# Kernel tuning notes

Hardware: AMD Instinct MI355X
Metric: run time of the kernel (lower is better)

Reference implementation:

```python
import jax, jax.numpy as jnp
import numpy as np

VOCAB, D_MODEL, N_STATE, H_HEADS, LAYERS = 64, 512, 32, 16, 4
EXPAND = 2
D_INNER = EXPAND * D_MODEL          # 1024
P_HEAD = D_INNER // H_HEADS         # 64
CONV_DIM = D_INNER + 2 * N_STATE    # x, B, C share the depthwise conv
K_CONV = 4
D_IN_PROJ = 2 * D_INNER + 2 * N_STATE + H_HEADS  # z, x, B, C, dt
BATCH, SEQ = 4, 1024
EPS = 1e-5


def rmsnorm(x, w):
    return x * jax.lax.rsqrt(jnp.mean(x * x, axis=-1, keepdims=True) + EPS) * w


def silu(x):
    return x * jax.nn.sigmoid(x)


def causal_depthwise_conv(x, w, b):
    # x: [B,L,C], w: [C,K], b: [C]; causal (left) padding, depthwise groups
    xt = jnp.transpose(x, (0, 2, 1))  # [B,C,L]
    out = jax.lax.conv_general_dilated(xt, w[:, None, :], (1,), [(K_CONV - 1, 0)], feature_group_count=w.shape[0])
    return jnp.transpose(out, (0, 2, 1)) + b


def ssd(xh, dt, A, Bm, Cm, Dp):
    # Mamba2 SSD recurrence. xh [B,L,H,P], dt [B,L,H], A [H], Bm/Cm [B,L,N], Dp [H]
    dA = jnp.exp(dt * A)              # decay per (batch, step, head)
    dtx = dt[..., None] * xh          # [B,L,H,P]

    def step(h, inp):
        dA_t, dtx_t, B_t, C_t = inp
        # h: [B,H,P,N]
        h = dA_t[:, :, None, None] * h + dtx_t[..., None] * B_t[:, None, None, :]
        y = jnp.einsum('bhpn,bn->bhp', h, C_t)
        return h, y

    h0 = jnp.zeros((xh.shape[0], H_HEADS, P_HEAD, N_STATE), xh.dtype)
    _, ys = jax.lax.scan(step, h0, (jnp.moveaxis(dA, 1, 0), jnp.moveaxis(dtx, 1, 0), jnp.moveaxis(Bm, 1, 0), jnp.moveaxis(Cm, 1, 0)))
    return jnp.moveaxis(ys, 0, 1) + xh * Dp[None, None, :, None]


def mamba_block(x, norm_w, W_in, b_in, conv_w, conv_b, dt_bias, A_log, Dp, gnorm_w, W_out, b_out):
    res = x
    u = rmsnorm(x, norm_w)
    zxbcdt = u @ W_in + b_in                                # [B,L,D_IN_PROJ]
    z = zxbcdt[..., :D_INNER]
    xBC = zxbcdt[..., D_INNER:D_INNER + CONV_DIM]
    dt = zxbcdt[..., D_INNER + CONV_DIM:]                   # [B,L,H]
    xBC = silu(causal_depthwise_conv(xBC, conv_w, conv_b))
    xc = xBC[..., :D_INNER]
    Bm = xBC[..., D_INNER:D_INNER + N_STATE]
    Cm = xBC[..., D_INNER + N_STATE:]
    dt = jax.nn.softplus(dt + dt_bias)
    xh = xc.reshape(xc.shape[0], xc.shape[1], H_HEADS, P_HEAD)
    y = ssd(xh, dt, -jnp.exp(A_log), Bm, Cm, Dp)
    y = y.reshape(y.shape[0], y.shape[1], D_INNER)
    y = rmsnorm(y * silu(z), gnorm_w)                       # gated RMSNorm
    return res + y @ W_out + b_out


def forward(input_tokens, emb, norm_w, W_in, b_in, conv_w, conv_b, dt_bias, A_log, D_param, gnorm_w, W_out, b_out, head_w, head_b):
    h = emb[input_tokens]
    for i in range(LAYERS):
        h = mamba_block(h, norm_w[i], W_in[i], b_in[i], conv_w[i], conv_b[i], dt_bias[i], A_log[i], D_param[i], gnorm_w[i], W_out[i], b_out[i])
    return h @ head_w + head_b


def setup_inputs() -> dict:
    key = jax.random.key(0)
    ks = jax.random.split(key, 8)
    s = 0.02
    return {
        'input_tokens': jax.random.randint(ks[0], (BATCH, SEQ), 0, VOCAB),
        'emb': jax.random.normal(ks[1], (VOCAB, D_MODEL), jnp.float32) * s,
        'norm_w': jnp.ones((LAYERS, D_MODEL), jnp.float32),
        'W_in': jax.random.normal(ks[2], (LAYERS, D_MODEL, D_IN_PROJ), jnp.float32) * s,
        'b_in': jnp.zeros((LAYERS, D_IN_PROJ), jnp.float32),
        'conv_w': jax.random.normal(ks[3], (LAYERS, CONV_DIM, K_CONV), jnp.float32) * 0.1,
        'conv_b': jnp.zeros((LAYERS, CONV_DIM), jnp.float32),
        'dt_bias': jnp.tile(jnp.log(jnp.expm1(jnp.linspace(0.001, 0.1, H_HEADS, dtype=jnp.float32))), (LAYERS, 1)),
        'A_log': jnp.tile(jnp.log(jnp.arange(1, H_HEADS + 1, dtype=jnp.float32)), (LAYERS, 1)),
        'D_param': jnp.ones((LAYERS, H_HEADS), jnp.float32),
        'gnorm_w': jnp.ones((LAYERS, D_INNER), jnp.float32),
        'W_out': jax.random.normal(ks[4], (LAYERS, D_INNER, D_MODEL), jnp.float32) * s,
        'b_out': jnp.zeros((LAYERS, D_MODEL), jnp.float32),
        'head_w': jax.random.normal(ks[5], (D_MODEL, VOCAB), jnp.float32) * s,
        'head_b': jnp.zeros((VOCAB,), jnp.float32),
    }


def reference(input_tokens, emb, norm_w, W_in, b_in, conv_w, conv_b, dt_bias, A_log, D_param, gnorm_w, W_out, b_out, head_w, head_b):
    return forward(input_tokens, emb, norm_w, W_in, b_in, conv_w, conv_b, dt_bias, A_log, D_param, gnorm_w, W_out, b_out, head_w, head_b)
```

## Files before the change

### kernel.cpp

```cpp
#include <hip/hip_runtime.h>
#include <hip/hip_bf16.h>

#define VOCAB     64
#define D_MODEL   512
#define N_STATE   32
#define H_HEADS   16
#define LAYERS    4
#define D_INNER   1024
#define P_HEAD    64
#define CONV_DIM  1088
#define K_CONV    4
#define D_IN_PROJ 2128
#define NPAD_IN   2176
#define NPAD_HEAD 64
#define BATCH     4
#define SEQ       1024
#define NTOK      (BATCH*SEQ)
#define EPS       1e-5f
#define CL        64
#define NC        (SEQ/CL)
#define PSTR      80

typedef __bf16 bf16x8 __attribute__((ext_vector_type(8)));
typedef float  f32x4  __attribute__((ext_vector_type(4)));

__device__ __forceinline__ float sigmoidf_(float x) { return 1.f / (1.f + __expf(-x)); }
__device__ __forceinline__ float softplusf_(float x) { return (x > 20.f) ? x : log1pf(__expf(x)); }

__device__ __forceinline__ void gload_lds16(const void* g, void* l) {
  __builtin_amdgcn_global_load_lds((const __attribute__((address_space(1))) void*)g,
                                   (__attribute__((address_space(3))) void*)l,
                                   16, 0, 0);
}

__device__ __forceinline__ int xcd_lin() {
  return (blockIdx.x & 7) * ((int)gridDim.x >> 3) + ((int)blockIdx.x >> 3);
}

__global__ __launch_bounds__(256) void embed_kernel(
    const int* __restrict__ tok, const float* __restrict__ emb,
    float* __restrict__ h, __bf16* __restrict__ hbf) {
  int wv = threadIdx.x >> 6, lane = threadIdx.x & 63;
  int tokid = blockIdx.x * 4 + wv;
  const float* er = emb + (size_t)tok[tokid] * D_MODEL;
  f32x4 v0 = *(const f32x4*)(er + lane * 8);
  f32x4 v1 = *(const f32x4*)(er + lane * 8 + 4);
  float* hr = h + (size_t)tokid * D_MODEL;
  *(f32x4*)(hr + lane * 8) = v0;
  *(f32x4*)(hr + lane * 8 + 4) = v1;
  bf16x8 o8;
  #pragma unroll
  for (int k = 0; k < 4; k++) { o8[k] = (__bf16)v0[k]; o8[4 + k] = (__bf16)v1[k]; }
  *(bf16x8*)(hbf + (size_t)tokid * D_MODEL + lane * 8) = o8;
}

__global__ __launch_bounds__(256) void transpose_all_kernel(
    const float* __restrict__ W_in, const float* __restrict__ W_out,
    const float* __restrict__ head_w,
    const float* __restrict__ norm_w, const float* __restrict__ gnorm_w,
    __bf16* __restrict__ WtIn, __bf16* __restrict__ WtOut, __bf16* __restrict__ WtHead) {
  int b = blockIdx.x;
  const float* W; const float* fold; __bf16* Wt; int K, N, Npad, bx, by;
  if (b < 4352) {
    int z = b / 1088, r = b % 1088;
    bx = r % 68; by = r / 68;
    W = W_in + (size_t)z * D_MODEL * D_IN_PROJ;
    fold = norm_w + (size_t)z * D_MODEL;
    Wt = WtIn + (size_t)z * NPAD_IN * D_MODEL;
    K = D_MODEL; N = D_IN_PROJ; Npad = NPAD_IN;
  } else if (b < 6400) {
    int r = b - 4352; int z = r / 512; r %= 512;
    bx = r % 16; by = r / 16;
    W = W_out + (size_t)z * D_INNER * D_MODEL;
    fold = gnorm_w + (size_t)z * D_INNER;
    Wt = WtOut + (size_t)z * D_MODEL * D_INNER;
    K = D_INNER; N = D_MODEL; Npad = D_MODEL;
  } else {
    int r = b - 6400;
    bx = r % 2; by = r / 2;
    W = head_w; fold = nullptr; Wt = WtHead;
    K = D_MODEL; N = VOCAB; Npad = NPAD_HEAD;
  }
  __shared__ float T[32][33];
  int n0 = bx * 32, k0 = by * 32;
  int tx = threadIdx.x & 31, ty = threadIdx.x >> 5;
  #pragma unroll
  for (int i = 0; i < 4; i++) {
    int n = n0 + tx;
    T[ty + i * 8][tx] = (n < N) ? W[(size_t)(k0 + ty + i * 8) * N + n] : 0.f;
  }
  __syncthreads();
  float fs = fold ? fold[k0 + tx] : 1.f;
  #pragma unroll
  for (int i = 0; i < 4; i++)
    Wt[(size_t)(n0 + ty + i * 8) * K + k0 + tx] = (__bf16)(T[tx][ty + i * 8] * fs);
}

#define TK 64
__global__ __launch_bounds__(256) void gemm64_kernel(
    const __bf16* __restrict__ A, const __bf16* __restrict__ Bt,
    const float* __restrict__ bias, const float* __restrict__ res,
    float* __restrict__ C, __bf16* __restrict__ Cbf,
    float inv_norm_dim, int nbx, int K, int N, int ldc) {
  __shared__ __bf16 As[2][64 * TK];
  __shared__ __bf16 Bs[2][64 * TK];
  int tid = threadIdx.x;
  int lane = tid & 63, wave = tid >> 6;
  int wm = wave >> 1, wn = wave & 1;
  int q = lane >> 4, l16 = lane & 15;
  int lin = xcd_lin();
  int bx = lin % nbx, by = lin / nbx;
  size_t row0 = (size_t)by * 64;
  int col0 = bx * 64;
  const __bf16* Ab = A + row0 * K;
  const __bf16* Bb = Bt + (size_t)col0 * K;

  auto stage = [&](int buf, int kk) {
    #pragma unroll
    for (int r = 0; r < 2; r++) {
      int lin2 = r * 256 + tid;
      size_t goff = (size_t)(lin2 >> 3) * K + kk + (lin2 & 7) * 8;
      gload_lds16(Ab + goff, &As[buf][lin2 * 8]);
      gload_lds16(Bb + goff, &Bs[buf][lin2 * 8]);
    }
  };

  f32x4 acc[2][2];
  #pragma unroll
  for (int i = 0; i < 2; i++)
    #pragma unroll
    for (int j = 0; j < 2; j++) acc[i][j] = (f32x4){0.f, 0.f, 0.f, 0.f};
  float ssqa[2] = {0.f, 0.f};

  stage(0, 0);
  int cur = 0;
  for (int k0 = 0; k0 < K; k0 += TK) {
    if (k0 + TK < K) {
      stage(cur ^ 1, k0 + TK);
      asm volatile("s_waitcnt vmcnt(4)" ::: "memory");
    } else {
      asm volatile("s_waitcnt vmcnt(0)" ::: "memory");
    }
    __builtin_amdgcn_s_barrier();
    #pragma unroll
    for (int ks = 0; ks < 2; ks++) {
      bf16x8 af[2], bfv[2];
      #pragma unroll
      for (int i = 0; i < 2; i++) {
        af[i] = *(const bf16x8*)(&As[cur][(wm * 32 + i * 16 + l16) * TK + ks * 32 + q * 8]);
        #pragma unroll
        for (int k = 0; k < 8; k++) { float v = (float)af[i][k]; ssqa[i] += v * v; }
      }
      #pragma unroll
      for (int j = 0; j < 2; j++)
        bfv[j] = *(const bf16x8*)(&Bs[cur][(wn * 32 + j * 16 + l16) * TK + ks * 32 + q * 8]);
      #pragma unroll
      for (int i = 0; i < 2; i++)
        #pragma unroll
        for (int j = 0; j < 2; j++)
          acc[i][j] = __builtin_amdgcn_mfma_f32_16x16x32_bf16(af[i], bfv[j], acc[i][j], 0, 0, 0);
    }
    __builtin_amdgcn_s_barrier();
    cur ^= 1;
  }

  #pragma unroll
  for (int i = 0; i < 2; i++) {
    ssqa[i] += __shfl_xor(ssqa[i], 16);
    ssqa[i] += __shfl_xor(ssqa[i], 32);
  }
  #pragma unroll
  for (int i = 0; i < 2; i++) {
    #pragma unroll
    for (int rr = 0; rr < 4; rr++) {
      size_t mrow = row0 + wm * 32 + i * 16 + q * 4 + rr;
      float sq = __shfl(ssqa[i], q * 4 + rr);
      float sc = (inv_norm_dim > 0.f) ? rsqrtf(sq * inv_norm_dim + EPS) : 1.f;
      #pragma unroll
      for (int j = 0; j < 2; j++) {
        int col = col0 + wn * 32 + j * 16 + l16;
        if (col < N) {
          size_t off = mrow * (size_t)ldc + col;
          float v = acc[i][j][rr] * sc + (bias ? bias[col] : 0.f);
          if (res) v += res[off];
          if (C)   C[off] = v;
          if (Cbf) Cbf[off] = (__bf16)v;
        }
      }
    }
  }
}

__global__ __launch_bounds__(256) void gemm_in_kernel(
    const __bf16* __restrict__ A, const __bf16* __restrict__ Bt,
    const float* __restrict__ bias, __bf16* __restrict__ Cbf,
    int nbx, int K, int N, int ldc) {
  __shared__ __bf16 As[2][64 * TK];
  __shared__ __bf16 Bs[2][128 * TK];
  int tid = threadIdx.x;
  int lane = tid & 63, wave = tid >> 6;
  int wm = wave >> 1, wn = wave & 1;
  int q = lane >> 4, l16 = lane & 15;
  int lin = xcd_lin();
  int bx = lin % nbx, by = lin / nbx;
  size_t row0 = (size_t)by * 64;
  int col0 = bx * 128;
  const __bf16* Ab = A + row0 * K;
  const __bf16* Bb = Bt + (size_t)col0 * K;

  auto stage = [&](int buf, int kk) {
    #pragma unroll
    for (int r = 0; r < 2; r++) {
      int lin2 = r * 256 + tid;
      gload_lds16(Ab + (size_t)(lin2 >> 3) * K + kk + (lin2 & 7) * 8, &As[buf][lin2 * 8]);
    }
    #pragma unroll
    for (int r = 0; r < 4; r++) {
      int lin2 = r * 256 + tid;
      gload_lds16(Bb + (size_t)(lin2 >> 3) * K + kk + (lin2 & 7) * 8, &Bs[buf][lin2 * 8]);
    }
  };

  f32x4 acc[2][4];
  #pragma unroll
  for (int i = 0; i < 2; i++)
    #pragma unroll
    for (int j = 0; j < 4; j++) acc[i][j] = (f32x4){0.f, 0.f, 0.f, 0.f};
  float ssqa[2] = {0.f, 0.f};

  stage(0, 0);
  int cur = 0;
  for (int k0 = 0; k0 < K; k0 += TK) {
    if (k0 + TK < K) {
      stage(cur ^ 1, k0 + TK);
      asm volatile("s_waitcnt vmcnt(6)" ::: "memory");
    } else {
      asm volatile("s_waitcnt vmcnt(0)" ::: "memory");
    }
    __builtin_amdgcn_s_barrier();
    #pragma unroll
    for (int ks = 0; ks < 2; ks++) {
      bf16x8 af[2], bfv[4];
      #pragma unroll
      for (int i = 0; i < 2; i++) {
        af[i] = *(const bf16x8*)(&As[cur][(wm * 32 + i * 16 + l16) * TK + ks * 32 + q * 8]);
        #pragma unroll
        for (int k = 0; k < 8; k++) { float v = (float)af[i][k]; ssqa[i] += v * v; }
      }
      #pragma unroll
      for (int j = 0; j < 4; j++)
        bfv[j] = *(const bf16x8*)(&Bs[cur][(wn * 64 + j * 16 + l16) * TK + ks * 32 + q * 8]);
      #pragma unroll
      for (int i = 0; i < 2; i++)
        #pragma unroll
        for (int j = 0; j < 4; j++)
          acc[i][j] = __builtin_amdgcn_mfma_f32_16x16x32_bf16(af[i], bfv[j], acc[i][j], 0, 0, 0);
    }
    __builtin_amdgcn_s_barrier();
    cur ^= 1;
  }

  #pragma unroll
  for (int i = 0; i < 2; i++) {
    ssqa[i] += __shfl_xor(ssqa[i], 16);
    ssqa[i] += __shfl_xor(ssqa[i], 32);
  }
  #pragma unroll
  for (int i = 0; i < 2; i++) {
    #pragma unroll
    for (int rr = 0; rr < 4; rr++) {
      size_t mrow = row0 + wm * 32 + i * 16 + q * 4 + rr;
      float sq = __shfl(ssqa[i], q * 4 + rr);
      float sc = rsqrtf(sq * (1.f / D_MODEL) + EPS);
      #pragma unroll
      for (int j = 0; j < 4; j++) {
        int col = col0 + wn * 64 + j * 16 + l16;
        if (col < N)
          Cbf[mrow * (size_t)ldc + col] = (__bf16)(acc[i][j][rr] * sc + bias[col]);
      }
    }
  }
}

__device__ __forceinline__ void wave0_dt_cumsum(
    const __bf16* __restrict__ zxbf, const float* __restrict__ dt_bias,
    int b, int h, int t0, int tid, float* ldt, float* lcs) {
  if (tid < 64) {
    float dv = (float)zxbf[((size_t)(b * SEQ + t0 + tid)) * D_IN_PROJ + 2 * D_INNER + 2 * N_STATE + h]
               + dt_bias[h];
    float dtv = softplusf_(dv);
    float cs = dtv;
    #pragma unroll
    for (int off = 1; off < 64; off <<= 1) {
      float o = __shfl_up(cs, off);
      if (tid >= off) cs += o;
    }
    ldt[tid] = dtv;
    lcs[tid] = cs;
  }
}

__global__ __launch_bounds__(256) void ssd_local_kernel(
    const __bf16* __restrict__ zxbf, const float* __restrict__ conv_w,
    const float* __restrict__ conv_b, const float* __restrict__ dt_bias,
    const float* __restrict__ A_log,
    float* __restrict__ Slocal, float* __restrict__ dAprod) {
  int blk = xcd_lin();
  int c = blk % NC;
  int h = (blk / NC) % H_HEADS;
  int b = blk / (NC * H_HEADS);
  int tid = threadIdx.x;
  int lane = tid & 63, wave = tid >> 6;
  int q = lane >> 4, l16 = lane & 15;
  int t0 = c * CL;
  float A = -__expf(A_log[h]);
  __shared__ __bf16 rawbuf[68 * 64 + 68 * 32];
  __shared__ __bf16 lxT[64][PSTR];
  __shared__ __bf16 lBT[32][PSTR];
  __shared__ float ldt[64], lcs[64];
  __bf16* rawx = rawbuf;
  __bf16* rawB = rawbuf + 68 * 64;
  for (int i = tid; i < 68 * 8; i += 256) {
    int r = i >> 3, c0 = (i & 7) * 8;
    int gr = t0 - 3 + r;
    bf16x8 v;
    #pragma unroll
    for (int k = 0; k < 8; k++) v[k] = (__bf16)0.f;
    if (gr >= 0)
      v = *(const bf16x8*)(zxbf + ((size_t)(b * SEQ + gr)) * D_IN_PROJ + D_INNER + h * 64 + c0);
    *(bf16x8*)(rawx + r * 64 + c0) = v;
  }
  for (int i = tid; i < 68 * 4; i += 256) {
    int r = i >> 2, c0 = (i & 3) * 8;
    int gr = t0 - 3 + r;
    bf16x8 v;
    #pragma unroll
    for (int k = 0; k < 8; k++) v[k] = (__bf16)0.f;
    if (gr >= 0)
      v = *(const bf16x8*)(zxbf + ((size_t)(b * SEQ + gr)) * D_IN_PROJ + 2 * D_INNER + c0);
    *(bf16x8*)(rawB + r * 32 + c0) = v;
  }
  wave0_dt_cumsum(zxbf, dt_bias, b, h, t0, tid, ldt, lcs);
  __syncthreads();
  float cs63 = lcs[63];
  {
    int p = tid & 63;
    const float* w = conv_w + (h * 64 + p) * K_CONV;
    float w0 = w[0], w1 = w[1], w2 = w[2], w3 = w[3];
    float cb = conv_b[h * 64 + p];
    for (int i = tid; i < CL * 64; i += 256) {
      int t = i >> 6;
      float a = cb + w0 * (float)rawx[t * 64 + p] + w1 * (float)rawx[(t + 1) * 64 + p]
                   + w2 * (float)rawx[(t + 2) * 64 + p] + w3 * (float)rawx[(t + 3) * 64 + p];
      lxT[p][t] = (__bf16)(a * sigmoidf_(a));
    }
  }
  {
    int n = tid & 31;
    const float* w = conv_w + (D_INNER + n) * K_CONV;
    float w0 = w[0], w1 = w[1], w2 = w[2], w3 = w[3];
    float cb = conv_b[D_INNER + n];
    for (int i = tid; i < CL * 32; i += 256) {
      int t = i >> 5;
      float a = cb + w0 * (float)rawB[t * 32 + n] + w1 * (float)rawB[(t + 1) * 32 + n]
                   + w2 * (float)rawB[(t + 2) * 32 + n] + w3 * (float)rawB[(t + 3) * 32 + n];
      float v = a * sigmoidf_(a);
      float wt = ldt[t] * __expf(A * (cs63 - lcs[t]));
      lBT[n][t] = (__bf16)(v * wt);
    }
  }
  __syncthreads();
  f32x4 acc[2];
  acc[0] = (f32x4){0.f,0.f,0.f,0.f}; acc[1] = (f32x4){0.f,0.f,0.f,0.f};
  #pragma unroll
  for (int kb = 0; kb < 2; kb++) {
    bf16x8 af = *(const bf16x8*)(&lxT[wave * 16 + l16][kb * 32 + q * 8]);
    #pragma unroll
    for (int j = 0; j < 2; j++) {
      bf16x8 bf = *(const bf16x8*)(&lBT[l16 + 16 * j][kb * 32 + q * 8]);
      acc[j] = __builtin_amdgcn_mfma_f32_16x16x32_bf16(af, bf, acc[j], 0, 0, 0);
    }
  }
  float* sT = (float*)rawbuf;
  #pragma unroll
  for (int j = 0; j < 2; j++) {
    int n = l16 + 16 * j;
    #pragma unroll
    for (int rr = 0; rr < 4; rr++) {
      int p = wave * 16 + q * 4 + rr;
      sT[p * 36 + n] = acc[j][rr];
    }
  }
  {
    int row = tid >> 2, c0 = (tid & 3) * 8;
    f32x4 a = *(const f32x4*)(sT + row * 36 + c0);
    f32x4 b2 = *(const f32x4*)(sT + row * 36 + c0 + 4);
    float* dstp = Slocal + (size_t)blk * 2048 + row * 32 + c0;
    *(f32x4*)dstp = a;
    *(f32x4*)(dstp + 4) = b2;
  }
  if (tid == 0) dAprod[blk] = __expf(A * cs63);
}

__global__ __launch_bounds__(256) void ssd_out_kernel(
    const __bf16* __restrict__ zxbf, const float* __restrict__ conv_w,
    const float* __restrict__ conv_b, const float* __restrict__ dt_bias,
    const float* __restrict__ A_log, const float* __restrict__ Dp,
    const float* __restrict__ Slocal, const float* __restrict__ dAprod,
    __bf16* __restrict__ gout) {
  int blk = xcd_lin();
  int c = blk % NC;
  int h = (blk / NC) % H_HEADS;
  int b = blk / (NC * H_HEADS);
  int tid = threadIdx.x;
  int lane = tid & 63, wave = tid >> 6;
  int q = lane >> 4, l16 = lane & 15;
  int t0 = c * CL;
  float A = -__expf(A_log[h]);
  float D = Dp[h];
  __shared__ __bf16 rawbuf[2 * 68 * 64];
  __shared__ __bf16 lxT[64][PSTR];
  __shared__ __bf16 lB[64][32];
  __shared__ __bf16 lC[64][32];
  __shared__ __bf16 lS[64][32];
  __shared__ float ldt[64], lcs[64];
  __shared__ float pr[NC];
  __bf16* rawx = rawbuf;
  __bf16* rawBC = rawbuf + 68 * 64;
  for (int i = tid; i < 68 * 8; i += 256) {
    int r = i >> 3, c0 = (i & 7) * 8;
    int gr = t0 - 3 + r;
    bf16x8 vx, vbc;
    #pragma unroll
    for (int k = 0; k < 8; k++) { vx[k] = (__bf16)0.f; vbc[k] = (__bf16)0.f; }
    if (gr >= 0) {
      const __bf16* rowp = zxbf + ((size_t)(b * SEQ + gr)) * D_IN_PROJ;
      vx  = *(const bf16x8*)(rowp + D_INNER + h * 64 + c0);
      vbc = *(const bf16x8*)(rowp + 2 * D_INNER + c0);
    }
    *(bf16x8*)(rawx + r * 64 + c0)  = vx;
    *(bf16x8*)(rawBC + r * 64 + c0) = vbc;
  }
  if (tid < NC) pr[tid] = dAprod[(blk - c) + tid];
  wave0_dt_cumsum(zxbf, dt_bias, b, h, t0, tid, ldt, lcs);
  __syncthreads();
  {
    int p = tid & 63;
    const float* w = conv_w + (h * 64 + p) * K_CONV;
    float w0 = w[0], w1 = w[1], w2 = w[2], w3 = w[3];
    float cb = conv_b[h * 64 + p];
    for (int i = tid; i < CL * 64; i += 256) {
      int t = i >> 6;
      float a = cb + w0 * (float)rawx[t * 64 + p] + w1 * (float)rawx[(t + 1) * 64 + p]
                   + w2 * (float)rawx[(t + 2) * 64 + p] + w3 * (float)rawx[(t + 3) * 64 + p];
      lxT[p][t] = (__bf16)(a * sigmoidf_(a));
    }
  }
  {
    int col = tid & 63;
    const float* w = conv_w + (D_INNER + col) * K_CONV;
    float w0 = w[0], w1 = w[1], w2 = w[2], w3 = w[3];
    float cb = conv_b[D_INNER + col];
    for (int i = tid; i < CL * 64; i += 256) {
      int t = i >> 6;
      float a = cb + w0 * (float)rawBC[t * 64 + col] + w1 * (float)rawBC[(t + 1) * 64 + col]
                   + w2 * (float)rawBC[(t + 2) * 64 + col] + w3 * (float)rawBC[(t + 3) * 64 + col];
      float v = a * sigmoidf_(a);
      if (col < 32) lB[t][col] = (__bf16)v; else lC[t][col - 32] = (__bf16)v;
    }
  }
  {
    int p = tid >> 2, n0 = (tid & 3) * 8;
    const float* sl = Slocal + (size_t)(blk - c) * 2048 + p * 32 + n0;
    float st[8] = {};
    for (int j = 0; j < c; j++) {
      f32x4 a = *(const f32x4*)(sl + (size_t)j * 2048);
      f32x4 bq = *(const f32x4*)(sl + (size_t)j * 2048 + 4);
      float prj = pr[j];
      #pragma unroll
      for (int k = 0; k < 4; k++) { st[k] = prj * st[k] + a[k]; st[4 + k] = prj * st[4 + k] + bq[k]; }
    }
    #pragma unroll
    for (int k = 0; k < 8; k++) lS[p][n0 + k] = (__bf16)st[k];
  }
  __syncthreads();
  bf16x8 afC = *(const bf16x8*)(&lC[wave * 16 + l16][q * 8]);
  f32x4 accG[4], accI[4], accY[4];
  #pragma unroll
  for (int j = 0; j < 4; j++) {
    accG[j] = (f32x4){0.f,0.f,0.f,0.f};
    accI[j] = (f32x4){0.f,0.f,0.f,0.f};
    accY[j] = (f32x4){0.f,0.f,0.f,0.f};
  }
  #pragma unroll
  for (int j = 0; j < 4; j++) {
    bf16x8 bf = *(const bf16x8*)(&lB[l16 + 16 * j][q * 8]);
    accG[j] = __builtin_amdgcn_mfma_f32_16x16x32_bf16(afC, bf, accG[j], 0, 0, 0);
  }
  #pragma unroll
  for (int j = 0; j < 4; j++) {
    bf16x8 bf = *(const bf16x8*)(&lS[l16 + 16 * j][q * 8]);
    accI[j] = __builtin_amdgcn_mfma_f32_16x16x32_bf16(afC, bf, accI[j], 0, 0, 0);
  }
  __bf16* pP = rawbuf + wave * 16 * PSTR;
  #pragma unroll
  for (int j = 0; j < 4; j++) {
    int s = l16 + 16 * j;
    float css = lcs[s], dts = ldt[s];
    #pragma unroll
    for (int rr = 0; rr < 4; rr++) {
      int tl = q * 4 + rr;
      int t = wave * 16 + tl;
      float val = accG[j][rr] * __expf(A * (lcs[t] - css)) * dts;
      if (s == t) val += D;
      if (s > t) val = 0.f;
      pP[tl * PSTR + s] = (__bf16)val;
    }
  }
  #pragma unroll
  for (int kb = 0; kb < 2; kb++) {
    bf16x8 afP = *(const bf16x8*)(pP + l16 * PSTR + kb * 32 + q * 8);
    #pragma unroll
    for (int j = 0; j < 4; j++) {
      bf16x8 bf = *(const bf16x8*)(&lxT[l16 + 16 * j][kb * 32 + q * 8]);
      accY[j] = __builtin_amdgcn_mfma_f32_16x16x32_bf16(afP, bf, accY[j], 0, 0, 0);
    }
  }
  __syncthreads();
  __bf16* yT = rawbuf;
  #pragma unroll
  for (int rr = 0; rr < 4; rr++) {
    int t = wave * 16 + q * 4 + rr;
    float cumt = __expf(A * lcs[t]);
    #pragma unroll
    for (int j = 0; j < 4; j++) {
      int p = l16 + 16 * j;
      yT[t * 72 + p] = (__bf16)(accY[j][rr] + cumt * accI[j][rr]);
    }
  }
  {
    int row = tid >> 2, col0 = (tid & 3) * 16;
    bf16x8 y0 = *(const bf16x8*)(yT + row * 72 + col0);
    bf16x8 y1 = *(const bf16x8*)(yT + row * 72 + col0 + 8);
    const __bf16* zrow = zxbf + ((size_t)(b * SEQ + t0 + row)) * D_IN_PROJ + h * 64 + col0;
    bf16x8 z0 = *(const bf16x8*)zrow;
    bf16x8 z1 = *(const bf16x8*)(zrow + 8);
    bf16x8 g0, g1;
    #pragma unroll
    for (int k = 0; k < 8; k++) {
      float zz = (float)z0[k];
      g0[k] = (__bf16)((float)y0[k] * zz * sigmoidf_(zz));
    }
    #pragma unroll
    for (int k = 0; k < 8; k++) {
      float zz = (float)z1[k];
      g1[k] = (__bf16)((float)y1[k] * zz * sigmoidf_(zz));
    }
    __bf16* grow = gout + ((size_t)(b * SEQ + t0 + row)) * D_INNER + h * 64 + col0;
    *(bf16x8*)grow = g0;
    *(bf16x8*)(grow + 8) = g1;
  }
}

extern "C" void kernel_launch(void* const* d_in, const int* in_sizes, int n_in,
                              void* d_out, int out_size, void* d_ws, size_t ws_size,
                              hipStream_t stream) {
  const int*   tok     = (const int*)  d_in[0];
  const float* emb     = (const float*)d_in[1];
  const float* norm_w  = (const float*)d_in[2];
  const float* W_in    = (const float*)d_in[3];
  const float* b_in    = (const float*)d_in[4];
  const float* conv_w  = (const float*)d_in[5];
  const float* conv_b  = (const float*)d_in[6];
  const float* dt_bias = (const float*)d_in[7];
  const float* A_log   = (const float*)d_in[8];
  const float* D_par   = (const float*)d_in[9];
  const float* gnorm_w = (const float*)d_in[10];
  const float* W_out   = (const float*)d_in[11];
  const float* b_out   = (const float*)d_in[12];
  const float* head_w  = (const float*)d_in[13];
  const float* head_b  = (const float*)d_in[14];
  float* out = (float*)d_out;

  char* p = (char*)d_ws;
  auto alloc = [&](size_t bytes) { void* r = (void*)p; p += (bytes + 255) & ~(size_t)255; return r; };
  float*  h      = (float*) alloc((size_t)NTOK * D_MODEL * 4);
  float*  slocal = (float*) alloc((size_t)BATCH * H_HEADS * NC * P_HEAD * N_STATE * 4);
  float*  daprod = (float*) alloc((size_t)BATCH * H_HEADS * NC * 4);
  __bf16* zxbf   = (__bf16*)alloc((size_t)NTOK * D_IN_PROJ * 2);
  __bf16* gbf    = (__bf16*)alloc((size_t)NTOK * D_INNER * 2);
  __bf16* hbf    = (__bf16*)alloc((size_t)NTOK * D_MODEL * 2);
  __bf16* WtIn   = (__bf16*)alloc((size_t)LAYERS * NPAD_IN * D_MODEL * 2);
  __bf16* WtOut  = (__bf16*)alloc((size_t)LAYERS * D_MODEL * D_INNER * 2);
  __bf16* WtHead = (__bf16*)alloc((size_t)NPAD_HEAD * D_MODEL * 2);

  transpose_all_kernel<<<6432, 256, 0, stream>>>(
      W_in, W_out, head_w, norm_w, gnorm_w, WtIn, WtOut, WtHead);

  embed_kernel<<<NTOK / 4, 256, 0, stream>>>(tok, emb, h, hbf);

  for (int l = 0; l < LAYERS; l++) {
    gemm_in_kernel<<<1088, 256, 0, stream>>>(
        hbf, WtIn + (size_t)l * NPAD_IN * D_MODEL, b_in + (size_t)l * D_IN_PROJ,
        zxbf, NPAD_IN / 128, D_MODEL, D_IN_PROJ, D_IN_PROJ);

    ssd_local_kernel<<<BATCH * H_HEADS * NC, 256, 0, stream>>>(
        zxbf, conv_w + (size_t)l * CONV_DIM * K_CONV, conv_b + (size_t)l * CONV_DIM,
        dt_bias + (size_t)l * H_HEADS, A_log + (size_t)l * H_HEADS, slocal, daprod);
    ssd_out_kernel<<<BATCH * H_HEADS * NC, 256, 0, stream>>>(
        zxbf, conv_w + (size_t)l * CONV_DIM * K_CONV, conv_b + (size_t)l * CONV_DIM,
        dt_bias + (size_t)l * H_HEADS, A_log + (size_t)l * H_HEADS,
        D_par + (size_t)l * H_HEADS, slocal, daprod, gbf);

    gemm64_kernel<<<512, 256, 0, stream>>>(
        gbf, WtOut + (size_t)l * D_MODEL * D_INNER, b_out + (size_t)l * D_MODEL, h,
        h, hbf, 1.f / D_INNER, D_MODEL / 64, D_INNER, D_MODEL, D_MODEL);
  }

  gemm64_kernel<<<64, 256, 0, stream>>>(
      hbf, WtHead, head_b, nullptr, out, nullptr, 0.f, 1, D_MODEL, VOCAB, VOCAB);
}
```

Baseline: 471.1 us.

## Fuse SSD local-state and output kernels with inter-block flag synchronisation

Merges the chunk-local state kernel and the output kernel into one launch, so the conv and SiLU on x, B and C and the raw loads run once instead of twice. Each block publishes its chunk state and decay product through a per-layer flag array using release/acquire atomics, and later chunks spin-wait on earlier chunks' flags. The flags are zeroed inside the embed kernel. This removes a kernel launch and the duplicated loads and conv work. It relies on blocks of earlier chunks being scheduled before they are waited on, which risks stalls or deadlock if residency is insufficient.

```diff
diff --git a/kernel.cpp b/kernel.cpp
--- a/kernel.cpp
+++ b/kernel.cpp
@@ -39,9 +39,13 @@
 
 __global__ __launch_bounds__(256) void embed_kernel(
     const int* __restrict__ tok, const float* __restrict__ emb,
-    float* __restrict__ h, __bf16* __restrict__ hbf) {
+    float* __restrict__ h, __bf16* __restrict__ hbf, float* __restrict__ flagsf) {
   int wv = threadIdx.x >> 6, lane = threadIdx.x & 63;
   int tokid = blockIdx.x * 4 + wv;
+  if (threadIdx.x == 0) {
+    #pragma unroll
+    for (int l = 0; l < LAYERS; l++) flagsf[l * 1024 + blockIdx.x] = 0.f;
+  }
   const float* er = emb + (size_t)tok[tokid] * D_MODEL;
   f32x4 v0 = *(const f32x4*)(er + lane * 8);
   f32x4 v1 = *(const f32x4*)(er + lane * 8 + 4);
@@ -300,11 +304,12 @@
   }
 }
 
-__global__ __launch_bounds__(256) void ssd_local_kernel(
+__global__ __launch_bounds__(256) void ssd_fused_kernel(
     const __bf16* __restrict__ zxbf, const float* __restrict__ conv_w,
     const float* __restrict__ conv_b, const float* __restrict__ dt_bias,
-    const float* __restrict__ A_log,
-    float* __restrict__ Slocal, float* __restrict__ dAprod) {
+    const float* __restrict__ A_log, const float* __restrict__ Dp,
+    float* __restrict__ Slocal, float* __restrict__ flagsf,
+    __bf16* __restrict__ gout) {
   int blk = xcd_lin();
   int c = blk % NC;
   int h = (blk / NC) % H_HEADS;
@@ -314,31 +319,30 @@
   int q = lane >> 4, l16 = lane & 15;
   int t0 = c * CL;
   float A = -__expf(A_log[h]);
-  __shared__ __bf16 rawbuf[68 * 64 + 68 * 32];
+  float D = Dp[h];
+  __shared__ __bf16 rawbuf[2 * 68 * 64];
   __shared__ __bf16 lxT[64][PSTR];
-  __shared__ __bf16 lBT[32][PSTR];
+  __shared__ __bf16 lBTw[32][PSTR];
+  __shared__ __bf16 lB[64][32];
+  __shared__ __bf16 lC[64][32];
+  __shared__ __bf16 lS[64][32];
   __shared__ float ldt[64], lcs[64];
+  __shared__ float pr[NC];
   __bf16* rawx = rawbuf;
-  __bf16* rawB = rawbuf + 68 * 64;
+  __bf16* rawBC = rawbuf + 68 * 64;
   for (int i = tid; i < 68 * 8; i += 256) {
     int r = i >> 3, c0 = (i & 7) * 8;
     int gr = t0 - 3 + r;
-    bf16x8 v;
-    #pragma unroll
-    for (int k = 0; k < 8; k++) v[k] = (__bf16)0.f;
-    if (gr >= 0)
-      v = *(const bf16x8*)(zxbf + ((size_t)(b * SEQ + gr)) * D_IN_PROJ + D_INNER + h * 64 + c0);
-    *(bf16x8*)(rawx + r * 64 + c0) = v;
-  }
-  for (int i = tid; i < 68 * 4; i += 256) {
-    int r = i >> 2, c0 = (i & 3) * 8;
-    int gr = t0 - 3 + r;
-    bf16x8 v;
-    #pragma unroll
-    for (int k = 0; k < 8; k++) v[k] = (__bf16)0.f;
-    if (gr >= 0)
-      v = *(const bf16x8*)(zxbf + ((size_t)(b * SEQ + gr)) * D_IN_PROJ + 2 * D_INNER + c0);
-    *(bf16x8*)(rawB + r * 32 + c0) = v;
+    bf16x8 vx, vbc;
+    #pragma unroll
+    for (int k = 0; k < 8; k++) { vx[k] = (__bf16)0.f; vbc[k] = (__bf16)0.f; }
+    if (gr >= 0) {
+      const __bf16* rowp = zxbf + ((size_t)(b * SEQ + gr)) * D_IN_PROJ;
+      vx  = *(const bf16x8*)(rowp + D_INNER + h * 64 + c0);
+      vbc = *(const bf16x8*)(rowp + 2 * D_INNER + c0);
+    }
+    *(bf16x8*)(rawx + r * 64 + c0)  = vx;
+    *(bf16x8*)(rawBC + r * 64 + c0) = vbc;
   }
   wave0_dt_cumsum(zxbf, dt_bias, b, h, t0, tid, ldt, lcs);
   __syncthreads();
@@ -356,107 +360,6 @@
     }
   }
   {
-    int n = tid & 31;
-    const float* w = conv_w + (D_INNER + n) * K_CONV;
-    float w0 = w[0], w1 = w[1], w2 = w[2], w3 = w[3];
-    float cb = conv_b[D_INNER + n];
-    for (int i = tid; i < CL * 32; i += 256) {
-      int t = i >> 5;
-      float a = cb + w0 * (float)rawB[t * 32 + n] + w1 * (float)rawB[(t + 1) * 32 + n]
-                   + w2 * (float)rawB[(t + 2) * 32 + n] + w3 * (float)rawB[(t + 3) * 32 + n];
-      float v = a * sigmoidf_(a);
-      float wt = ldt[t] * __expf(A * (cs63 - lcs[t]));
-      lBT[n][t] = (__bf16)(v * wt);
-    }
-  }
-  __syncthreads();
-  f32x4 acc[2];
-  acc[0] = (f32x4){0.f,0.f,0.f,0.f}; acc[1] = (f32x4){0.f,0.f,0.f,0.f};
-  #pragma unroll
-  for (int kb = 0; kb < 2; kb++) {
-    bf16x8 af = *(const bf16x8*)(&lxT[wave * 16 + l16][kb * 32 + q * 8]);
-    #pragma unroll
-    for (int j = 0; j < 2; j++) {
-      bf16x8 bf = *(const bf16x8*)(&lBT[l16 + 16 * j][kb * 32 + q * 8]);
-      acc[j] = __builtin_amdgcn_mfma_f32_16x16x32_bf16(af, bf, acc[j], 0, 0, 0);
-    }
-  }
-  float* sT = (float*)rawbuf;
-  #pragma unroll
-  for (int j = 0; j < 2; j++) {
-    int n = l16 + 16 * j;
-    #pragma unroll
-    for (int rr = 0; rr < 4; rr++) {
-      int p = wave * 16 + q * 4 + rr;
-      sT[p * 36 + n] = acc[j][rr];
-    }
-  }
-  {
-    int row = tid >> 2, c0 = (tid & 3) * 8;
-    f32x4 a = *(const f32x4*)(sT + row * 36 + c0);
-    f32x4 b2 = *(const f32x4*)(sT + row * 36 + c0 + 4);
-    float* dstp = Slocal + (size_t)blk * 2048 + row * 32 + c0;
-    *(f32x4*)dstp = a;
-    *(f32x4*)(dstp + 4) = b2;
-  }
-  if (tid == 0) dAprod[blk] = __expf(A * cs63);
-}
-
-__global__ __launch_bounds__(256) void ssd_out_kernel(
-    const __bf16* __restrict__ zxbf, const float* __restrict__ conv_w,
-    const float* __restrict__ conv_b, const float* __restrict__ dt_bias,
-    const float* __restrict__ A_log, const float* __restrict__ Dp,
-    const float* __restrict__ Slocal, const float* __restrict__ dAprod,
-    __bf16* __restrict__ gout) {
-  int blk = xcd_lin();
-  int c = blk % NC;
-  int h = (blk / NC) % H_HEADS;
-  int b = blk / (NC * H_HEADS);
-  int tid = threadIdx.x;
-  int lane = tid & 63, wave = tid >> 6;
-  int q = lane >> 4, l16 = lane & 15;
-  int t0 = c * CL;
-  float A = -__expf(A_log[h]);
-  float D = Dp[h];
-  __shared__ __bf16 rawbuf[2 * 68 * 64];
-  __shared__ __bf16 lxT[64][PSTR];
-  __shared__ __bf16 lB[64][32];
-  __shared__ __bf16 lC[64][32];
-  __shared__ __bf16 lS[64][32];
-  __shared__ float ldt[64], lcs[64];
-  __shared__ float pr[NC];
-  __bf16* rawx = rawbuf;
-  __bf16* rawBC = rawbuf + 68 * 64;
-  for (int i = tid; i < 68 * 8; i += 256) {
-    int r = i >> 3, c0 = (i & 7) * 8;
-    int gr = t0 - 3 + r;
-    bf16x8 vx, vbc;
-    #pragma unroll
-    for (int k = 0; k < 8; k++) { vx[k] = (__bf16)0.f; vbc[k] = (__bf16)0.f; }
-    if (gr >= 0) {
-      const __bf16* rowp = zxbf + ((size_t)(b * SEQ + gr)) * D_IN_PROJ;
-      vx  = *(const bf16x8*)(rowp + D_INNER + h * 64 + c0);
-      vbc = *(const bf16x8*)(rowp + 2 * D_INNER + c0);
-    }
-    *(bf16x8*)(rawx + r * 64 + c0)  = vx;
-    *(bf16x8*)(rawBC + r * 64 + c0) = vbc;
-  }
-  if (tid < NC) pr[tid] = dAprod[(blk - c) + tid];
-  wave0_dt_cumsum(zxbf, dt_bias, b, h, t0, tid, ldt, lcs);
-  __syncthreads();
-  {
-    int p = tid & 63;
-    const float* w = conv_w + (h * 64 + p) * K_CONV;
-    float w0 = w[0], w1 = w[1], w2 = w[2], w3 = w[3];
-    float cb = conv_b[h * 64 + p];
-    for (int i = tid; i < CL * 64; i += 256) {
-      int t = i >> 6;
-      float a = cb + w0 * (float)rawx[t * 64 + p] + w1 * (float)rawx[(t + 1) * 64 + p]
-                   + w2 * (float)rawx[(t + 2) * 64 + p] + w3 * (float)rawx[(t + 3) * 64 + p];
-      lxT[p][t] = (__bf16)(a * sigmoidf_(a));
-    }
-  }
-  {
     int col = tid & 63;
     const float* w = conv_w + (D_INNER + col) * K_CONV;
     float w0 = w[0], w1 = w[1], w2 = w[2], w3 = w[3];
@@ -466,9 +369,57 @@
       float a = cb + w0 * (float)rawBC[t * 64 + col] + w1 * (float)rawBC[(t + 1) * 64 + col]
                    + w2 * (float)rawBC[(t + 2) * 64 + col] + w3 * (float)rawBC[(t + 3) * 64 + col];
       float v = a * sigmoidf_(a);
-      if (col < 32) lB[t][col] = (__bf16)v; else lC[t][col - 32] = (__bf16)v;
-    }
-  }
+      if (col < 32) {
+        lB[t][col] = (__bf16)v;
+        float wt = ldt[t] * __expf(A * (cs63 - lcs[t]));
+        lBTw[col][t] = (__bf16)(v * wt);
+      } else {
+        lC[t][col - 32] = (__bf16)v;
+      }
+    }
+  }
+  __syncthreads();
+  if (c < NC - 1) {
+    f32x4 acc0 = (f32x4){0.f,0.f,0.f,0.f}, acc1 = (f32x4){0.f,0.f,0.f,0.f};
+    #pragma unroll
+    for (int kb = 0; kb < 2; kb++) {
+      bf16x8 af = *(const bf16x8*)(&lxT[wave * 16 + l16][kb * 32 + q * 8]);
+      bf16x8 b0 = *(const bf16x8*)(&lBTw[l16][kb * 32 + q * 8]);
+      bf16x8 b1 = *(const bf16x8*)(&lBTw[l16 + 16][kb * 32 + q * 8]);
+      acc0 = __builtin_amdgcn_mfma_f32_16x16x32_bf16(af, b0, acc0, 0, 0, 0);
+      acc1 = __builtin_amdgcn_mfma_f32_16x16x32_bf16(af, b1, acc1, 0, 0, 0);
+    }
+    float* sT = (float*)rawbuf;
+    #pragma unroll
+    for (int rr = 0; rr < 4; rr++) {
+      int p = wave * 16 + q * 4 + rr;
+      sT[p * 36 + l16]      = acc0[rr];
+      sT[p * 36 + l16 + 16] = acc1[rr];
+    }
+    {
+      int row = tid >> 2, c0 = (tid & 3) * 8;
+      f32x4 a = *(const f32x4*)(sT + row * 36 + c0);
+      f32x4 b2 = *(const f32x4*)(sT + row * 36 + c0 + 4);
+      float* dstp = Slocal + (size_t)blk * 2048 + row * 32 + c0;
+      *(f32x4*)dstp = a;
+      *(f32x4*)(dstp + 4) = b2;
+    }
+    __syncthreads();
+    if (tid == 0) {
+      __threadfence();
+      __hip_atomic_store(&flagsf[blk], 1.f + __expf(A * cs63),
+                         __ATOMIC_RELEASE, __HIP_MEMORY_SCOPE_AGENT);
+    }
+  }
+  if (tid < c) {
+    float v = __hip_atomic_load(&flagsf[blk - c + tid], __ATOMIC_ACQUIRE, __HIP_MEMORY_SCOPE_AGENT);
+    while (v == 0.f) {
+      __builtin_amdgcn_s_sleep(2);
+      v = __hip_atomic_load(&flagsf[blk - c + tid], __ATOMIC_ACQUIRE, __HIP_MEMORY_SCOPE_AGENT);
+    }
+    pr[tid] = v - 1.f;
+  }
+  __syncthreads();
   {
     int p = tid >> 2, n0 = (tid & 3) * 8;
     const float* sl = Slocal + (size_t)(blk - c) * 2048 + p * 32 + n0;
@@ -586,7 +537,7 @@
   auto alloc = [&](size_t bytes) { void* r = (void*)p; p += (bytes + 255) & ~(size_t)255; return r; };
   float*  h      = (float*) alloc((size_t)NTOK * D_MODEL * 4);
   float*  slocal = (float*) alloc((size_t)BATCH * H_HEADS * NC * P_HEAD * N_STATE * 4);
-  float*  daprod = (float*) alloc((size_t)BATCH * H_HEADS * NC * 4);
+  float*  flags  = (float*) alloc((size_t)LAYERS * 1024 * 4);
   __bf16* zxbf   = (__bf16*)alloc((size_t)NTOK * D_IN_PROJ * 2);
   __bf16* gbf    = (__bf16*)alloc((size_t)NTOK * D_INNER * 2);
   __bf16* hbf    = (__bf16*)alloc((size_t)NTOK * D_MODEL * 2);
@@ -597,20 +548,17 @@
   transpose_all_kernel<<<6432, 256, 0, stream>>>(
       W_in, W_out, head_w, norm_w, gnorm_w, WtIn, WtOut, WtHead);
 
-  embed_kernel<<<NTOK / 4, 256, 0, stream>>>(tok, emb, h, hbf);
+  embed_kernel<<<NTOK / 4, 256, 0, stream>>>(tok, emb, h, hbf, flags);
 
   for (int l = 0; l < LAYERS; l++) {
     gemm_in_kernel<<<1088, 256, 0, stream>>>(
         hbf, WtIn + (size_t)l * NPAD_IN * D_MODEL, b_in + (size_t)l * D_IN_PROJ,
         zxbf, NPAD_IN / 128, D_MODEL, D_IN_PROJ, D_IN_PROJ);
 
-    ssd_local_kernel<<<BATCH * H_HEADS * NC, 256, 0, stream>>>(
-        zxbf, conv_w + (size_t)l * CONV_DIM * K_CONV, conv_b + (size_t)l * CONV_DIM,
-        dt_bias + (size_t)l * H_HEADS, A_log + (size_t)l * H_HEADS, slocal, daprod);
-    ssd_out_kernel<<<BATCH * H_HEADS * NC, 256, 0, stream>>>(
+    ssd_fused_kernel<<<BATCH * H_HEADS * NC, 256, 0, stream>>>(
         zxbf, conv_w + (size_t)l * CONV_DIM * K_CONV, conv_b + (size_t)l * CONV_DIM,
         dt_bias + (size_t)l * H_HEADS, A_log + (size_t)l * H_HEADS,
-        D_par + (size_t)l * H_HEADS, slocal, daprod, gbf);
+        D_par + (size_t)l * H_HEADS, slocal, flags + (size_t)l * 1024, gbf);
 
     gemm64_kernel<<<512, 256, 0, stream>>>(
         gbf, WtOut + (size_t)l * D_MODEL * D_INNER, b_out + (size_t)l * D_MODEL, h,
```

Result: slower. 705.1 us (+49.7%).
